# Kernel tuning notes

Measured on AMD Instinct MI355X. Metric: run time of the kernel, lower is better.

The kernel has to match this reference:

```python
import jax, jax.numpy as jnp
import numpy as np

EPS = 1e-6
GROUPS = 32


def group_norm(x, scale, bias):
    # x: [b, c, d, h, w]
    b, c, d, h, w = x.shape
    xg = x.reshape(b, GROUPS, c // GROUPS, d, h, w)
    mean = xg.mean(axis=(2, 3, 4, 5), keepdims=True)
    var = xg.var(axis=(2, 3, 4, 5), keepdims=True)
    xn = ((xg - mean) * jax.lax.rsqrt(var + EPS)).reshape(b, c, d, h, w)
    return xn * scale[None, :, None, None, None] + bias[None, :, None, None, None]


def setup_inputs() -> dict:
    key = jax.random.key(0)
    ks = jax.random.split(key, 6)
    C = 512
    x = jax.random.normal(ks[0], (2, C, 16, 16, 16), dtype=jnp.float32)
    s = 1.0 / np.sqrt(C)
    return {
        "x": x,
        "gn_scale": jnp.ones((C,), jnp.float32),
        "gn_bias": jnp.zeros((C,), jnp.float32),
        "wq": jax.random.normal(ks[1], (C, C), jnp.float32) * s,
        "bq": jnp.zeros((C,), jnp.float32),
        "wk": jax.random.normal(ks[2], (C, C), jnp.float32) * s,
        "bk": jnp.zeros((C,), jnp.float32),
        "wv": jax.random.normal(ks[3], (C, C), jnp.float32) * s,
        "bv": jnp.zeros((C,), jnp.float32),
        "wproj": jax.random.normal(ks[4], (C, C), jnp.float32) * s,
        "bproj": jnp.zeros((C,), jnp.float32),
    }


def reference(x, gn_scale, gn_bias, wq, bq, wk, bk, wv, bv, wproj, bproj):
    b, c, d, h, w = x.shape
    h_ = group_norm(x, gn_scale, gn_bias)
    hf = h_.reshape(b, c, d * h * w)  # [b, c, N]
    # 1x1x1 convs == per-position channel matmuls
    q = jnp.einsum("oc,bcn->bon", wq, hf) + bq[None, :, None]
    k = jnp.einsum("oc,bcn->bon", wk, hf) + bk[None, :, None]
    v = jnp.einsum("oc,bcn->bon", wv, hf) + bv[None, :, None]
    # attn[b, i, j] = softmax_j(q_i . k_j / sqrt(c))
    attn = jnp.einsum("bci,bcj->bij", q, k) * (c ** -0.5)
    attn = jax.nn.softmax(attn, axis=-1)
    # out[b, c, i] = sum_j v[b, c, j] * attn[b, i, j]
    out = jnp.einsum("bcj,bij->bci", v, attn)
    out = jnp.einsum("oc,bcn->bon", wproj, out) + bproj[None, :, None]
    return x + out.reshape(b, c, d, h, w)
```

## Files before the change

kernel.cpp:

```cpp
#include <hip/hip_runtime.h>
#include <hip/hip_bf16.h>

#define BB 2
#define CC 512
#define GG 32
#define NN 4096
#define EPSV 1e-6f

typedef __attribute__((ext_vector_type(4))) float f32x4;
typedef __attribute__((ext_vector_type(8))) short s16x8;
typedef __attribute__((ext_vector_type(4))) short s16x4;

__device__ __forceinline__ ushort f2bf(float f){
  union { float f; unsigned u; } v; v.f = f;
  unsigned r = v.u + 0x7fffu + ((v.u >> 16) & 1u);
  return (ushort)(r >> 16);
}
__device__ __forceinline__ short f2bfs(float f){ return (short)f2bf(f); }
__device__ __forceinline__ float b2f(ushort u){
  union { unsigned u; float f; } v; v.u = ((unsigned)u) << 16; return v.f;
}

__device__ __forceinline__ f32x4 mfma16(s16x8 a, s16x8 b, f32x4 c){
  return __builtin_amdgcn_mfma_f32_16x16x32_bf16(a, b, c, 0, 0, 0);
}

#define GLOAD_LDS16(g, l) __builtin_amdgcn_global_load_lds( \
    (const __attribute__((address_space(1))) void*)(g),     \
    (__attribute__((address_space(3))) void*)(l), 16, 0, 0)

__global__ __launch_bounds__(256) void k_convert_w(const float* __restrict__ wq, const float* __restrict__ wk,
                                                   const float* __restrict__ wv, const float* __restrict__ wp,
                                                   ushort* __restrict__ wbf){
  int idx = blockIdx.x * 256 + threadIdx.x;
  const float* srcs[4] = {wq, wk, wv, wp};
  #pragma unroll
  for (int m = 0; m < 4; m++){
    float4 v = reinterpret_cast<const float4*>(srcs[m])[idx];
    ushort4 o; o.x = f2bf(v.x); o.y = f2bf(v.y); o.z = f2bf(v.z); o.w = f2bf(v.w);
    reinterpret_cast<ushort4*>(wbf + (size_t)m * CC * CC)[idx] = o;
  }
}

__global__ __launch_bounds__(256) void k_gn_stats1(const float* __restrict__ x, float* __restrict__ pstat){
  int blk = blockIdx.x;
  const float* p = x + (size_t)blk * 16384;
  float s = 0.f, ss = 0.f;
  for (int i = threadIdx.x; i < 4096; i += 256){
    float4 v = reinterpret_cast<const float4*>(p)[i];
    s  += v.x + v.y + v.z + v.w;
    ss += v.x*v.x + v.y*v.y + v.z*v.z + v.w*v.w;
  }
  #pragma unroll
  for (int off = 32; off; off >>= 1){ s += __shfl_down(s, off); ss += __shfl_down(ss, off); }
  __shared__ float rs_[4], rss_[4];
  int w = threadIdx.x >> 6, lane = threadIdx.x & 63;
  if (lane == 0){ rs_[w] = s; rss_[w] = ss; }
  __syncthreads();
  if (threadIdx.x == 0){
    pstat[blk * 2 + 0] = rs_[0] + rs_[1] + rs_[2] + rs_[3];
    pstat[blk * 2 + 1] = rss_[0] + rss_[1] + rss_[2] + rss_[3];
  }
}
__global__ __launch_bounds__(64) void k_gn_stats2(const float* __restrict__ pstat, float* __restrict__ stats){
  int bg = blockIdx.x;
  int l = threadIdx.x;
  float s = 0.f, ss = 0.f;
  if (l < 4){ s = pstat[(bg * 4 + l) * 2]; ss = pstat[(bg * 4 + l) * 2 + 1]; }
  #pragma unroll
  for (int off = 2; off; off >>= 1){ s += __shfl_down(s, off); ss += __shfl_down(ss, off); }
  if (l == 0){
    float inv = 1.0f / (16.0f * NN);
    float mean = s * inv;
    float var = ss * inv - mean * mean;
    stats[bg * 2 + 0] = mean;
    stats[bg * 2 + 1] = rsqrtf(var + EPSV);
  }
}

__global__ __launch_bounds__(256) void k_gn_apply(const float* __restrict__ x, const float* __restrict__ gsc,
                                                  const float* __restrict__ gbi, const float* __restrict__ stats,
                                                  ushort* __restrict__ hf){
  __shared__ ushort tr[32][520];
  int b = blockIdx.y;
  int nb = blockIdx.x * 32;
  int t = threadIdx.x;
  int n = t & 31, cr = t >> 5;
  const float* xb = x + (size_t)b * CC * NN;
  for (int c0 = 0; c0 < CC; c0 += 8){
    int c = c0 + cr;
    float mean = stats[(b * GG + (c >> 4)) * 2 + 0];
    float rstd = stats[(b * GG + (c >> 4)) * 2 + 1];
    float v = xb[(size_t)c * NN + nb + n];
    tr[n][c] = f2bf((v - mean) * rstd * gsc[c] + gbi[c]);
  }
  __syncthreads();
  ushort* out = hf + ((size_t)b * NN + nb) * CC;
  int c8 = (t & 63) * 8;
  int nrow0 = t >> 6;
  #pragma unroll
  for (int i = 0; i < 8; i++){
    int nr = nrow0 + i * 4;
    *reinterpret_cast<s16x8*>(&out[(size_t)nr * CC + c8]) =
      *reinterpret_cast<const s16x8*>(&tr[nr][c8]);
  }
}

__global__ __launch_bounds__(256, 3) void k_gemm_qkv2(const ushort* __restrict__ W, const ushort* __restrict__ Bt,
                                                      const float* __restrict__ bq, const float* __restrict__ bk,
                                                      const float* __restrict__ bv,
                                                      ushort* __restrict__ qo, ushort* __restrict__ ko,
                                                      ushort* __restrict__ vo, float rs){
  __shared__ __align__(16) char smem[40960];
  __shared__ float bl[3][64];
  int b = blockIdx.z, ob = blockIdx.y * 64, nb = blockIdx.x * 128;
  int t = threadIdx.x, w = t >> 6, l = t & 63;
  int lr = l & 15, lk = l >> 4;
  int wo = (w >> 1) * 32, wn = (w & 1) * 64;
  if (t < 64){ bl[0][t] = bq[ob + t]; bl[1][t] = bk[ob + t]; bl[2][t] = bv[ob + t]; }
  const ushort* Bp = Bt + ((size_t)b * NN + nb) * CC;
  const ushort* Wp = W + (size_t)ob * CC;
  int srow = l >> 2;
  int schunk = (l & 3) ^ ((l >> 2) & 3) ^ ((l >> 4) & 3);
  int xs = (lk ^ (lr & 3) ^ ((lr >> 2) & 3)) * 8;

#define STAGE_QKV(BUF, K0)                                                               \
  {                                                                                      \
    ushort* As_ = (ushort*)(smem + (BUF) * 20480);                                       \
    ushort* Bs_ = As_ + 6144;                                                            \
    _Pragma("unroll")                                                                    \
    for (int tt = 0; tt < 5; tt++){                                                      \
      int inst = w * 5 + tt;                                                             \
      if (inst < 12){                                                                    \
        int m = inst >> 2, sub = inst & 3;                                               \
        const ushort* src = Wp + (size_t)m * CC * CC + (size_t)(sub * 16 + srow) * CC + (K0) + schunk * 8; \
        GLOAD_LDS16(src, As_ + m * 2048 + sub * 512);                                    \
      } else {                                                                           \
        int q = inst - 12;                                                               \
        const ushort* src = Bp + (size_t)(q * 16 + srow) * CC + (K0) + schunk * 8;       \
        GLOAD_LDS16(src, Bs_ + q * 512);                                                 \
      }                                                                                  \
    }                                                                                    \
  }

  f32x4 acc[3][2][4] = {};
  STAGE_QKV(0, 0)
  __syncthreads();
  for (int s16 = 0; s16 < 16; s16++){
    if (s16 < 15) STAGE_QKV((s16 + 1) & 1, (s16 + 1) * 32)
    const ushort* As = (const ushort*)(smem + (s16 & 1) * 20480);
    const ushort* Bs = As + 6144;
    s16x8 bf[4];
    #pragma unroll
    for (int sn = 0; sn < 4; sn++)
      bf[sn] = *(const s16x8*)&Bs[(wn + sn * 16 + lr) * 32 + xs];
    #pragma unroll
    for (int m = 0; m < 3; m++){
      s16x8 a0 = *(const s16x8*)&As[m * 2048 + (wo + lr) * 32 + xs];
      s16x8 a1 = *(const s16x8*)&As[m * 2048 + (wo + 16 + lr) * 32 + xs];
      #pragma unroll
      for (int sn = 0; sn < 4; sn++){
        acc[m][0][sn] = mfma16(a0, bf[sn], acc[m][0][sn]);
        acc[m][1][sn] = mfma16(a1, bf[sn], acc[m][1][sn]);
      }
    }
    __syncthreads();
  }
#undef STAGE_QKV
  #pragma unroll
  for (int m = 0; m < 2; m++){
    ushort* dst = (m == 0) ? qo : ko;
    float scl = (m == 0) ? rs : 1.0f;
    #pragma unroll
    for (int so = 0; so < 2; so++)
      #pragma unroll
      for (int sn = 0; sn < 4; sn++){
        int o0 = wo + so * 16 + lk * 4;
        int n  = nb + wn + sn * 16 + lr;
        s16x4 pv;
        #pragma unroll
        for (int r = 0; r < 4; r++) pv[r] = f2bfs((acc[m][so][sn][r] + bl[m][o0 + r]) * scl);
        *reinterpret_cast<s16x4*>(&dst[((size_t)b * NN + n) * CC + ob + o0]) = pv;
      }
  }
  ushort* Ve = (ushort*)smem;
  #pragma unroll
  for (int so = 0; so < 2; so++)
    #pragma unroll
    for (int sn = 0; sn < 4; sn++){
      int o0 = wo + so * 16 + lk * 4;
      int ncl = wn + sn * 16 + lr;
      #pragma unroll
      for (int r = 0; r < 4; r++) Ve[(o0 + r) * 136 + ncl] = f2bf(acc[2][so][sn][r] + bl[2][o0 + r]);
    }
  __syncthreads();
  {
    int row = t >> 2, cs = (t & 3) * 32;
    ushort* dst = &vo[((size_t)b * CC + ob + row) * NN + nb + cs];
    #pragma unroll
    for (int k = 0; k < 4; k++)
      *(s16x8*)&dst[k * 8] = *(const s16x8*)&Ve[row * 136 + cs + k * 8];
  }
}

__global__ __launch_bounds__(512, 2) void k_gemm_s(const ushort* __restrict__ qt, const ushort* __restrict__ kt,
                                                   ushort* __restrict__ P, float* __restrict__ part){
  extern __shared__ __align__(16) char smem[];
  int lin = blockIdx.x + 16 * blockIdx.y + 256 * blockIdx.z;
  int tt0 = (lin & 7) * 64 + (lin >> 3);
  int jblk = tt0 & 15;
  int pair = tt0 >> 4;
  int b = pair >> 4;
  int j0 = jblk * 256, i0 = (pair & 15) * 256;
  int t = threadIdx.x, w = t >> 6, l = t & 63;
  int lr = l & 15, lk = l >> 4;
  int wj2 = w >> 2, wi4 = w & 3;
  const ushort* kb = kt + ((size_t)b * NN + j0) * CC;
  const ushort* qb = qt + ((size_t)b * NN + i0) * CC;
  int srow = l >> 3;
  int schunk = (l & 7) ^ srow;

#define STAGE_S(BUF, K0)                                                          \
  {                                                                               \
    ushort* Ks_ = (ushort*)(smem + (BUF) * 32768);                                \
    ushort* Qs_ = (ushort*)(smem + 65536 + (BUF) * 32768);                        \
    _Pragma("unroll")                                                             \
    for (int tt = 0; tt < 8; tt++){                                               \
      int inst = w * 8 + tt;                                                      \
      if (inst < 32){                                                             \
        const ushort* src = kb + (size_t)(inst * 8 + srow) * CC + (K0) + schunk * 8; \
        GLOAD_LDS16(src, Ks_ + inst * 512);                                       \
      } else {                                                                    \
        int g = inst - 32;                                                        \
        const ushort* src = qb + (size_t)(g * 8 + srow) * CC + (K0) + schunk * 8; \
        GLOAD_LDS16(src, Qs_ + g * 512);                                          \
      }                                                                           \
    }                                                                             \
  }

  f32x4 acc[8][4] = {};
  STAGE_S(0, 0)
  for (int s8 = 0; s8 < 8; s8++){
    if (s8 < 7){
      STAGE_S((s8 + 1) & 1, (s8 + 1) * 64)
      asm volatile("s_waitcnt vmcnt(8)" ::: "memory");
    } else {
      asm volatile("s_waitcnt vmcnt(0)" ::: "memory");
    }
    __builtin_amdgcn_s_barrier();
    __builtin_amdgcn_sched_barrier(0);
    const ushort* Ks = (const ushort*)(smem + (s8 & 1) * 32768);
    const ushort* Qs = (const ushort*)(smem + 65536 + (s8 & 1) * 32768);
    #pragma unroll
    for (int kk = 0; kk < 2; kk++){
      int xs = ((kk * 4 + lk) ^ (lr & 7)) * 8;
      s16x8 bf[4];
      #pragma unroll
      for (int si = 0; si < 4; si++)
        bf[si] = *(const s16x8*)&Qs[(wi4 * 64 + si * 16 + lr) * 64 + xs];
      #pragma unroll
      for (int sj = 0; sj < 8; sj++){
        s16x8 a = *(const s16x8*)&Ks[(wj2 * 128 + sj * 16 + lr) * 64 + xs];
        #pragma unroll
        for (int si = 0; si < 4; si++)
          acc[sj][si] = mfma16(a, bf[si], acc[sj][si]);
      }
    }
    asm volatile("s_waitcnt lgkmcnt(0)" ::: "memory");
    __builtin_amdgcn_s_barrier();
    __builtin_amdgcn_sched_barrier(0);
  }
#undef STAGE_S
  ushort* Pe = (ushort*)smem;
  float rsum[4] = {0.f, 0.f, 0.f, 0.f};
  #pragma unroll
  for (int pass = 0; pass < 2; pass++){
    if ((wi4 >> 1) == pass){
      #pragma unroll
      for (int sj = 0; sj < 8; sj++)
        #pragma unroll
        for (int si = 0; si < 4; si++){
          int il = (wi4 & 1) * 64 + si * 16 + lr;
          int jl = wj2 * 128 + sj * 16 + lk * 4;
          s16x4 pk;
          #pragma unroll
          for (int r = 0; r < 4; r++){
            float e = __builtin_amdgcn_exp2f(acc[sj][si][r]);
            pk[r] = f2bfs(e);
            rsum[si] += e;
          }
          *(s16x4*)&Pe[il * 264 + jl] = pk;
        }
    }
    __syncthreads();
    {
      int row = t >> 2, cs = (t & 3) * 64;
      ushort* dst = P + ((size_t)b * NN + i0 + pass * 128 + row) * NN + j0 + cs;
      #pragma unroll
      for (int k = 0; k < 8; k++)
        *(s16x8*)&dst[k * 8] = *(const s16x8*)&Pe[row * 264 + cs + k * 8];
    }
    __syncthreads();
  }
  #pragma unroll
  for (int si = 0; si < 4; si++){
    float s = rsum[si];
    s += __shfl_xor(s, 16);
    s += __shfl_xor(s, 32);
    if (lk == 0){
      int il = wi4 * 64 + si * 16 + lr;
      part[((size_t)b * NN + i0 + il) * 32 + jblk * 2 + wj2] = s;
    }
  }
}

__global__ __launch_bounds__(256) void k_rowsum2(const float* __restrict__ part, float* __restrict__ linv){
  int row = blockIdx.x * 4 + (threadIdx.x >> 6);
  int l = threadIdx.x & 63;
  float s = (l < 32) ? part[(size_t)row * 32 + l] : 0.f;
  #pragma unroll
  for (int off = 32; off; off >>= 1) s += __shfl_down(s, off);
  if (l == 0) linv[row] = 1.0f / s;
}

__global__ __launch_bounds__(512) void k_gemm_o(const ushort* __restrict__ P, const ushort* __restrict__ vv,
                                                const float* __restrict__ linv, ushort* __restrict__ ot){
  __shared__ __align__(16) char smem[65536];
  int lin = blockIdx.x + 4 * blockIdx.y + 128 * blockIdx.z;
  int tt0 = (lin & 7) * 32 + (lin >> 3);
  int cblk = tt0 & 3;
  int ib   = tt0 >> 2;
  int b = ib >> 5;
  int c0 = cblk * 128, i0 = (ib & 31) * 128;
  int t = threadIdx.x, w = t >> 6, l = t & 63;
  int lr = l & 15, lk = l >> 4;
  int wi2 = w >> 2, wc4 = w & 3;
  const ushort* vb = vv + ((size_t)b * CC + c0) * NN;
  const ushort* pb = P + ((size_t)b * NN + i0) * NN;
  int srow = l >> 3;
  int schunk = (l & 7) ^ srow;

#define STAGE_O(BUF, K0)                                                          \
  {                                                                               \
    ushort* Vs_ = (ushort*)(smem + (BUF) * 16384);                                \
    ushort* Ps_ = (ushort*)(smem + 32768 + (BUF) * 16384);                        \
    _Pragma("unroll")                                                             \
    for (int tt = 0; tt < 4; tt++){                                               \
      int inst = w * 4 + tt;                                                      \
      if (inst < 16){                                                             \
        const ushort* src = vb + (size_t)(inst * 8 + srow) * NN + (K0) + schunk * 8; \
        GLOAD_LDS16(src, Vs_ + inst * 512);                                       \
      } else {                                                                    \
        int g = inst - 16;                                                        \
        const ushort* src = pb + (size_t)(g * 8 + srow) * NN + (K0) + schunk * 8; \
        GLOAD_LDS16(src, Ps_ + g * 512);                                          \
      }                                                                           \
    }                                                                             \
  }

  f32x4 acc[2][4] = {};
  STAGE_O(0, 0)
  for (int s64 = 0; s64 < 64; s64++){
    if (s64 < 63){
      STAGE_O((s64 + 1) & 1, (s64 + 1) * 64)
      asm volatile("s_waitcnt vmcnt(4)" ::: "memory");
    } else {
      asm volatile("s_waitcnt vmcnt(0)" ::: "memory");
    }
    __builtin_amdgcn_s_barrier();
    __builtin_amdgcn_sched_barrier(0);
    const ushort* Vs = (const ushort*)(smem + (s64 & 1) * 16384);
    const ushort* Ps = (const ushort*)(smem + 32768 + (s64 & 1) * 16384);
    #pragma unroll
    for (int kk = 0; kk < 2; kk++){
      int xs = ((kk * 4 + lk) ^ (lr & 7)) * 8;
      s16x8 af[2], bf[4];
      #pragma unroll
      for (int sc = 0; sc < 2; sc++)
        af[sc] = *(const s16x8*)&Vs[(wc4 * 32 + sc * 16 + lr) * 64 + xs];
      #pragma unroll
      for (int si = 0; si < 4; si++)
        bf[si] = *(const s16x8*)&Ps[(wi2 * 64 + si * 16 + lr) * 64 + xs];
      #pragma unroll
      for (int sc = 0; sc < 2; sc++)
        #pragma unroll
        for (int si = 0; si < 4; si++)
          acc[sc][si] = mfma16(af[sc], bf[si], acc[sc][si]);
    }
    asm volatile("s_waitcnt lgkmcnt(0)" ::: "memory");
    __builtin_amdgcn_s_barrier();
    __builtin_amdgcn_sched_barrier(0);
  }
#undef STAGE_O
  ushort* Oe = (ushort*)smem;
  #pragma unroll
  for (int si = 0; si < 4; si++){
    int il = wi2 * 64 + si * 16 + lr;
    float li = linv[(size_t)b * NN + i0 + il];
    #pragma unroll
    for (int sc = 0; sc < 2; sc++){
      int cl = wc4 * 32 + sc * 16 + lk * 4;
      s16x4 pk;
      #pragma unroll
      for (int r = 0; r < 4; r++) pk[r] = f2bfs(acc[sc][si][r] * li);
      *(s16x4*)&Oe[il * 136 + cl] = pk;
    }
  }
  __syncthreads();
  {
    int row = t >> 2, cs = (t & 3) * 32;
    ushort* dst = ot + ((size_t)b * NN + i0 + row) * CC + c0 + cs;
    #pragma unroll
    for (int k = 0; k < 4; k++)
      *(s16x8*)&dst[k * 8] = *(const s16x8*)&Oe[row * 136 + cs + k * 8];
  }
}

__global__ __launch_bounds__(256, 3) void k_gemm_proj2(const ushort* __restrict__ A, const ushort* __restrict__ Bt,
                                                       const float* __restrict__ bias, float* __restrict__ o32,
                                                       const float* __restrict__ xres){
  __shared__ __align__(16) char smem[34048];
  __shared__ float bl[64];
  int b = blockIdx.z, ob = blockIdx.y * 64, nb = blockIdx.x * 128;
  int t = threadIdx.x, w = t >> 6, l = t & 63;
  int lr = l & 15, lk = l >> 4;
  int wo = (w >> 1) * 32, wn = (w & 1) * 64;
  if (t < 64) bl[t] = bias[ob + t];
  const ushort* Bp = Bt + ((size_t)b * NN + nb) * CC;
  const ushort* Ap = A + (size_t)ob * CC;
  int srow = l >> 2;
  int schunk = (l & 3) ^ ((l >> 2) & 3) ^ ((l >> 4) & 3);
  int xs = (lk ^ (lr & 3) ^ ((lr >> 2) & 3)) * 8;

#define STAGE_P2(BUF, K0)                                                         \
  {                                                                               \
    ushort* As_ = (ushort*)(smem + (BUF) * 12288);                                \
    ushort* Bs_ = As_ + 2048;                                                     \
    _Pragma("unroll")                                                             \
    for (int tt = 0; tt < 3; tt++){                                               \
      int inst = w * 3 + tt;                                                      \
      if (inst < 4){                                                              \
        const ushort* src = Ap + (size_t)(inst * 16 + srow) * CC + (K0) + schunk * 8; \
        GLOAD_LDS16(src, As_ + inst * 512);                                       \
      } else {                                                                    \
        int q = inst - 4;                                                         \
        const ushort* src = Bp + (size_t)(q * 16 + srow) * CC + (K0) + schunk * 8; \
        GLOAD_LDS16(src, Bs_ + q * 512);                                          \
      }                                                                           \
    }                                                                             \
  }

  f32x4 acc[2][4] = {};
  STAGE_P2(0, 0)
  __syncthreads();
  for (int s16 = 0; s16 < 16; s16++){
    if (s16 < 15) STAGE_P2((s16 + 1) & 1, (s16 + 1) * 32)
    const ushort* As = (const ushort*)(smem + (s16 & 1) * 12288);
    const ushort* Bs = As + 2048;
    s16x8 a0 = *(const s16x8*)&As[(wo + lr) * 32 + xs];
    s16x8 a1 = *(const s16x8*)&As[(wo + 16 + lr) * 32 + xs];
    #pragma unroll
    for (int sn = 0; sn < 4; sn++){
      s16x8 bf = *(const s16x8*)&Bs[(wn + sn * 16 + lr) * 32 + xs];
      acc[0][sn] = mfma16(a0, bf, acc[0][sn]);
      acc[1][sn] = mfma16(a1, bf, acc[1][sn]);
    }
    __syncthreads();
  }
#undef STAGE_P2
  float* trf = (float*)smem;
  #pragma unroll
  for (int so = 0; so < 2; so++)
    #pragma unroll
    for (int sn = 0; sn < 4; sn++){
      int o0 = wo + so * 16 + lk * 4;
      int ncl = wn + sn * 16 + lr;
      #pragma unroll
      for (int r = 0; r < 4; r++) trf[(o0 + r) * 133 + ncl] = acc[so][sn][r] + bl[o0 + r];
    }
  __syncthreads();
  {
    int row = t >> 2, cs = (t & 3) * 32;
    size_t base = ((size_t)b * CC + ob + row) * NN + nb + cs;
    #pragma unroll
    for (int q = 0; q < 8; q++){
      float4 xv = *reinterpret_cast<const float4*>(&xres[base + q * 4]);
      float4 ov;
      ov.x = xv.x + trf[row * 133 + cs + q * 4 + 0];
      ov.y = xv.y + trf[row * 133 + cs + q * 4 + 1];
      ov.z = xv.z + trf[row * 133 + cs + q * 4 + 2];
      ov.w = xv.w + trf[row * 133 + cs + q * 4 + 3];
      *reinterpret_cast<float4*>(&o32[base + q * 4]) = ov;
    }
  }
}

extern "C" void kernel_launch(void* const* d_in, const int* in_sizes, int n_in,
                              void* d_out, int out_size, void* d_ws, size_t ws_size,
                              hipStream_t stream){
  const float* x   = (const float*)d_in[0];
  const float* gsc = (const float*)d_in[1];
  const float* gbi = (const float*)d_in[2];
  const float* wq  = (const float*)d_in[3];
  const float* bq  = (const float*)d_in[4];
  const float* wk  = (const float*)d_in[5];
  const float* bk  = (const float*)d_in[6];
  const float* wv  = (const float*)d_in[7];
  const float* bv  = (const float*)d_in[8];
  const float* wp  = (const float*)d_in[9];
  const float* bp  = (const float*)d_in[10];
  char* ws = (char*)d_ws;
  const size_t MB = 1024 * 1024;
  ushort* wbf  = (ushort*)ws;
  ushort* qtb  = (ushort*)(ws + 2 * MB);
  ushort* ktb  = (ushort*)(ws + 10 * MB);
  ushort* vvb  = (ushort*)(ws + 18 * MB);
  ushort* hfb  = (ushort*)(ws + 26 * MB);
  ushort* Pbuf = (ushort*)(ws + 34 * MB);
  float* linv  = (float*)(ws + 98 * MB);
  float* stats = (float*)(ws + 98 * MB + 64 * 1024);
  float* pstat = (float*)(ws + 98 * MB + 96 * 1024);
  float* part  = (float*)(ws + 26 * MB);
  ushort* otb = hfb;

  const float rs = 0.044194173824159216f * 1.4426950408889634f;

  k_convert_w<<<256, 256, 0, stream>>>(wq, wk, wv, wp, wbf);
  k_gn_stats1<<<256, 256, 0, stream>>>(x, pstat);
  k_gn_stats2<<<64, 64, 0, stream>>>(pstat, stats);
  k_gn_apply<<<dim3(128, 2, 1), 256, 0, stream>>>(x, gsc, gbi, stats, hfb);
  k_gemm_qkv2<<<dim3(32, 8, 2), 256, 0, stream>>>(wbf, hfb, bq, bk, bv, qtb, ktb, vvb, rs);
  k_gemm_s<<<dim3(16, 16, 2), 512, 131072, stream>>>(qtb, ktb, Pbuf, part);
  k_rowsum2<<<2048, 256, 0, stream>>>(part, linv);
  k_gemm_o<<<dim3(4, 32, 2), 512, 0, stream>>>(Pbuf, vvb, linv, otb);
  k_gemm_proj2<<<dim3(32, 8, 2), 256, 0, stream>>>(wbf + 3 * CC * CC, otb, bp, (float*)d_out, x);
}
```

Measured before the change: 177.5 us.

## Interleave K/Q half-tile prefetch with MFMA phases in S-GEMM

Restructures the QK^T GEMM main loop into four phases per k-step. Each phase loads its K fragments, issues a half-tile global-to-LDS prefetch (next K tile, or the Q tile two steps ahead), then runs 16 MFMAs under raised priority. Q fragments are now loaded once per k-step and reused across all phases. The aim is to spread memory traffic across the compute so loads and MFMAs overlap better. The cost is more barriers per iteration and a more complex buffer-reuse schedule, where a missed wait-count could introduce a race.

```diff
diff --git a/kernel.cpp b/kernel.cpp
--- a/kernel.cpp
+++ b/kernel.cpp
@@ -220,57 +220,80 @@
   int srow = l >> 3;
   int schunk = (l & 7) ^ srow;
 
-#define STAGE_S(BUF, K0)                                                          \
+#define STAGE_KH(BUF, K0, H)                                                      \
   {                                                                               \
-    ushort* Ks_ = (ushort*)(smem + (BUF) * 32768);                                \
-    ushort* Qs_ = (ushort*)(smem + 65536 + (BUF) * 32768);                        \
+    ushort* D = (ushort*)(smem + (BUF) * 32768);                                  \
     _Pragma("unroll")                                                             \
-    for (int tt = 0; tt < 8; tt++){                                               \
-      int inst = w * 8 + tt;                                                      \
-      if (inst < 32){                                                             \
-        const ushort* src = kb + (size_t)(inst * 8 + srow) * CC + (K0) + schunk * 8; \
-        GLOAD_LDS16(src, Ks_ + inst * 512);                                       \
-      } else {                                                                    \
-        int g = inst - 32;                                                        \
-        const ushort* src = qb + (size_t)(g * 8 + srow) * CC + (K0) + schunk * 8; \
-        GLOAD_LDS16(src, Qs_ + g * 512);                                          \
-      }                                                                           \
+    for (int tt = 0; tt < 2; tt++){                                               \
+      int g = (H) * 16 + w * 2 + tt;                                              \
+      const ushort* src = kb + (size_t)(g * 8 + srow) * CC + (K0) + schunk * 8;   \
+      GLOAD_LDS16(src, D + g * 512);                                              \
     }                                                                             \
   }
+#define STAGE_QH(BUF, K0, H)                                                      \
+  {                                                                               \
+    ushort* D = (ushort*)(smem + 65536 + (BUF) * 32768);                          \
+    _Pragma("unroll")                                                             \
+    for (int tt = 0; tt < 2; tt++){                                               \
+      int g = (H) * 16 + w * 2 + tt;                                              \
+      const ushort* src = qb + (size_t)(g * 8 + srow) * CC + (K0) + schunk * 8;   \
+      GLOAD_LDS16(src, D + g * 512);                                              \
+    }                                                                             \
+  }
+#define PHASE(SJ, STAGE_CODE)                                                     \
+  {                                                                               \
+    s16x8 a00 = *(const s16x8*)&Ks[(wj2 * 128 + (SJ) * 16 + lr) * 64 + xs0];      \
+    s16x8 a01 = *(const s16x8*)&Ks[(wj2 * 128 + (SJ) * 16 + lr) * 64 + xs1];      \
+    s16x8 a10 = *(const s16x8*)&Ks[(wj2 * 128 + ((SJ) + 1) * 16 + lr) * 64 + xs0];\
+    s16x8 a11 = *(const s16x8*)&Ks[(wj2 * 128 + ((SJ) + 1) * 16 + lr) * 64 + xs1];\
+    STAGE_CODE                                                                    \
+    __builtin_amdgcn_s_barrier();                                                 \
+    asm volatile("s_waitcnt lgkmcnt(0)" ::: "memory");                            \
+    __builtin_amdgcn_sched_barrier(0);                                            \
+    __builtin_amdgcn_s_setprio(1);                                                \
+    _Pragma("unroll")                                                             \
+    for (int si = 0; si < 4; si++){                                               \
+      acc[SJ][si]       = mfma16(a00, bq[si][0], acc[SJ][si]);                    \
+      acc[SJ][si]       = mfma16(a01, bq[si][1], acc[SJ][si]);                    \
+      acc[(SJ) + 1][si] = mfma16(a10, bq[si][0], acc[(SJ) + 1][si]);              \
+      acc[(SJ) + 1][si] = mfma16(a11, bq[si][1], acc[(SJ) + 1][si]);              \
+    }                                                                             \
+    __builtin_amdgcn_s_setprio(0);                                                \
+    __builtin_amdgcn_s_barrier();                                                 \
+  }
 
   f32x4 acc[8][4] = {};
-  STAGE_S(0, 0)
+  STAGE_KH(0, 0, 0)
+  STAGE_KH(0, 0, 1)
+  STAGE_QH(0, 0, 0)
+  STAGE_QH(0, 0, 1)
+  STAGE_QH(1, 64, 0)
+  STAGE_QH(1, 64, 1)
+  #pragma unroll
   for (int s8 = 0; s8 < 8; s8++){
-    if (s8 < 7){
-      STAGE_S((s8 + 1) & 1, (s8 + 1) * 64)
-      asm volatile("s_waitcnt vmcnt(8)" ::: "memory");
-    } else {
-      asm volatile("s_waitcnt vmcnt(0)" ::: "memory");
-    }
+    const int tau = s8 & 1;
+    const ushort* Ks = (const ushort*)(smem + tau * 32768);
+    const ushort* Qs = (const ushort*)(smem + 65536 + tau * 32768);
+    if (s8 < 7){ asm volatile("s_waitcnt vmcnt(4)" ::: "memory"); }
+    else       { asm volatile("s_waitcnt vmcnt(0)" ::: "memory"); }
     __builtin_amdgcn_s_barrier();
     __builtin_amdgcn_sched_barrier(0);
-    const ushort* Ks = (const ushort*)(smem + (s8 & 1) * 32768);
-    const ushort* Qs = (const ushort*)(smem + 65536 + (s8 & 1) * 32768);
-    #pragma unroll
-    for (int kk = 0; kk < 2; kk++){
-      int xs = ((kk * 4 + lk) ^ (lr & 7)) * 8;
-      s16x8 bf[4];
-      #pragma unroll
-      for (int si = 0; si < 4; si++)
-        bf[si] = *(const s16x8*)&Qs[(wi4 * 64 + si * 16 + lr) * 64 + xs];
-      #pragma unroll
-      for (int sj = 0; sj < 8; sj++){
-        s16x8 a = *(const s16x8*)&Ks[(wj2 * 128 + sj * 16 + lr) * 64 + xs];
-        #pragma unroll
-        for (int si = 0; si < 4; si++)
-          acc[sj][si] = mfma16(a, bf[si], acc[sj][si]);
-      }
-    }
-    asm volatile("s_waitcnt lgkmcnt(0)" ::: "memory");
-    __builtin_amdgcn_s_barrier();
-    __builtin_amdgcn_sched_barrier(0);
-  }
-#undef STAGE_S
+    int xs0 = (lk ^ (lr & 7)) * 8;
+    int xs1 = ((4 + lk) ^ (lr & 7)) * 8;
+    s16x8 bq[4][2];
+    #pragma unroll
+    for (int si = 0; si < 4; si++){
+      bq[si][0] = *(const s16x8*)&Qs[(wi4 * 64 + si * 16 + lr) * 64 + xs0];
+      bq[si][1] = *(const s16x8*)&Qs[(wi4 * 64 + si * 16 + lr) * 64 + xs1];
+    }
+    PHASE(0, if (s8 < 7) STAGE_KH(tau ^ 1, (s8 + 1) * 64, 0))
+    PHASE(2, if (s8 < 7) STAGE_KH(tau ^ 1, (s8 + 1) * 64, 1))
+    PHASE(4, if (s8 < 6) STAGE_QH(tau, (s8 + 2) * 64, 0))
+    PHASE(6, if (s8 < 6) STAGE_QH(tau, (s8 + 2) * 64, 1))
+  }
+#undef PHASE
+#undef STAGE_KH
+#undef STAGE_QH
   ushort* Pe = (ushort*)smem;
   float rsum[4] = {0.f, 0.f, 0.f, 0.f};
   #pragma unroll
```

Measured after the change: 180.6 us. About the same (+1.8%).
